# Kernel optimization log

Measured on AMD Instinct MI355X. Metric: run time of the kernel, lower is better.

The kernel has to match this reference:

```python
import jax, jax.numpy as jnp
import numpy as np

B, N, K, D = 8, 4096, 16, 256


def layer_norm(x, g, b, eps=1e-5):
    m = jnp.mean(x, axis=-1, keepdims=True)
    v = jnp.var(x, axis=-1, keepdims=True)
    return (x - m) * jax.lax.rsqrt(v + eps) * g + b


def setup_inputs() -> dict:
    key = jax.random.key(0)
    ks = jax.random.split(key, 8)

    def lin(k, fi, fo):
        return (jax.random.normal(k, (fi, fo), jnp.float32) / np.sqrt(fi).astype(np.float32),
                jnp.zeros((fo,), jnp.float32))

    coordinates = jax.random.normal(ks[0], (B, N, 3), jnp.float32)
    W1, b1 = lin(ks[1], 10, D // 4)
    W2, b2 = lin(ks[2], D // 4, D // 2)
    W3, b3 = lin(ks[3], D // 2, D)
    Wa1, ba1 = lin(ks[4], D, D)
    Wa2, ba2 = lin(ks[5], D, D)
    return {
        'coordinates': coordinates,
        'W1': W1, 'b1': b1, 'g1': jnp.ones((D // 4,)), 'be1': jnp.zeros((D // 4,)),
        'W2': W2, 'b2': b2, 'g2': jnp.ones((D // 2,)), 'be2': jnp.zeros((D // 2,)),
        'W3': W3, 'b3': b3, 'g3': jnp.ones((D,)), 'be3': jnp.zeros((D,)),
        'Wa1': Wa1, 'ba1': ba1, 'ga1': jnp.ones((D,)), 'bea1': jnp.zeros((D,)),
        'Wa2': Wa2, 'ba2': ba2,
    }


def reference(coordinates, W1, b1, g1, be1, W2, b2, g2, be2, W3, b3, g3, be3,
              Wa1, ba1, ga1, bea1, Wa2, ba2):
    # kNN via squared-distance matrix (monotone in Euclidean distance)
    sq = jnp.sum(coordinates * coordinates, axis=-1)  # [B,N]
    d2 = sq[:, :, None] + sq[:, None, :] - 2.0 * jnp.einsum('bnd,bmd->bnm', coordinates, coordinates)
    _, idx = jax.lax.top_k(-d2, K)  # smallest K distances, [B,N,K]

    nbr = jax.vmap(lambda c, i: c[i])(coordinates, idx)  # [B,N,K,3]
    rel = nbr - coordinates[:, :, None, :]               # relative positions
    dist = jnp.linalg.norm(rel, axis=-1, keepdims=True)  # [B,N,K,1]
    rn = rel / (dist + 1e-6)
    axy = jnp.arctan2(rn[..., 1], rn[..., 0])[..., None]
    axz = jnp.arctan2(rn[..., 2], rn[..., 0])[..., None]
    ayz = jnp.arctan2(rn[..., 2], rn[..., 1])[..., None]
    geom = jnp.concatenate([dist, rel, axy, axz, ayz, rn], axis=-1)  # [B,N,K,10]

    # encoder MLP
    h = jax.nn.relu(layer_norm(geom @ W1 + b1, g1, be1))
    h = jax.nn.relu(layer_norm(h @ W2 + b2, g2, be2))
    h = layer_norm(h @ W3 + b3, g3, be3)

    agg = jnp.mean(h, axis=2)  # mean over neighbors -> [B,N,D]

    # aggregator MLP
    out = jax.nn.relu(layer_norm(agg @ Wa1 + ba1, ga1, bea1)) @ Wa2 + ba2
    return out
```

## Files before the change

### kernel.cpp

```cpp
#include <hip/hip_runtime.h>
#include <hip/hip_bf16.h>
#include <math.h>

#define BB 8
#define NN 4096
#define KK 16
#define DD 256

typedef __hip_bfloat16 bf16;
typedef _Float16 half8 __attribute__((ext_vector_type(8)));
typedef float f32x4 __attribute__((ext_vector_type(4)));

union HFU { _Float16 h; unsigned short u; };
__device__ __forceinline__ unsigned short f2h(float x) { HFU v; v.h = (_Float16)x; return v.u; }

#define CONV_TOTAL 273344
#define O_COORD 0
#define O_W1 98304
#define O_b1 98944
#define O_g1 99008
#define O_be1 99072
#define O_W2 99136
#define O_b2 107328
#define O_g2 107456
#define O_be2 107584
#define O_W3 107712
#define O_b3 140480
#define O_g3 140736
#define O_be3 140992
#define O_Wa1 141248
#define O_ba1 206784
#define O_ga1 207040
#define O_bea1 207296
#define O_Wa2 207552
#define O_ba2 273088

#define F_W1 0
#define F_W2 2048
#define F_W3 10240
#define F_A1 43008
#define F_A2 108544
#define FRAG_TOTAL 174080

struct SrcPtrs {
  const void* p[19];
};

__global__ __launch_bounds__(256) void convert_kernel(SrcPtrs sp, float* __restrict__ dst) {
  static constexpr int OFF[20] = {
      0,      98304,  98944,  99008,  99072,  99136,  107328, 107456, 107584,
      107712, 140480, 140736, 140992, 141248, 206784, 207040, 207296, 207552,
      273088, 273344};
  const int i = blockIdx.x * 256 + threadIdx.x;
  if (i >= CONV_TOTAL) return;
  const unsigned tag = ((const unsigned*)sp.p[3])[0];
  const bool isb = (tag == 0x3F803F80u);
  int s = 0;
#pragma unroll
  for (int j = 1; j < 19; j++)
    if (i >= OFF[j]) s = j;
  const int local = i - OFF[s];
  float v = isb ? __bfloat162float(((const bf16*)sp.p[s])[local])
                : ((const float*)sp.p[s])[local];
  dst[i] = v;
}

__global__ __launch_bounds__(256) void swizzle_kernel(const float* __restrict__ conv,
                                                      unsigned short* __restrict__ frag) {
  const int t = blockIdx.x * 256 + threadIdx.x;
  if (t >= FRAG_TOTAL) return;
  int l, e;
  if (t < 2048) { l = 0; e = t; }
  else if (t < 10240) { l = 1; e = t - 2048; }
  else if (t < 43008) { l = 2; e = t - 10240; }
  else if (t < 108544) { l = 3; e = t - 43008; }
  else { l = 4; e = t - 108544; }
  static constexpr int WOFF[5] = {O_W1, O_W2, O_W3, O_Wa1, O_Wa2};
  static constexpr int NDIM[5] = {64, 128, 256, 256, 256};
  static constexpr int NTC[5] = {4, 8, 16, 16, 16};
  static constexpr int KREAL[5] = {10, 64, 128, 256, 256};
  static constexpr int HOFF[5] = {F_W1, F_W2, F_W3, F_A1, F_A2};
  const int j = e & 7;
  const int lane = (e >> 3) & 63;
  const int tile = e >> 9;
  const int nt = tile % NTC[l];
  const int kt = tile / NTC[l];
  const int k = kt * 32 + (lane >> 4) * 8 + j;
  const int n = nt * 16 + (lane & 15);
  float w = (k < KREAL[l]) ? conv[WOFF[l] + k * NDIM[l] + n] : 0.0f;
  frag[HOFF[l] + e] = f2h(w);
}

__device__ __forceinline__ float sq3_rn(float x, float y, float z) {
  return __fadd_rn(__fadd_rn(__fmul_rn(x, x), __fmul_rn(y, y)), __fmul_rn(z, z));
}
__device__ __forceinline__ float dot3_rn(float ax, float ay, float az, float bx, float by, float bz) {
  return __fadd_rn(__fadd_rn(__fmul_rn(ax, bx), __fmul_rn(ay, by)), __fmul_rn(az, bz));
}
__device__ __forceinline__ unsigned f2ord(float f) {
  unsigned u = __float_as_uint(f);
  return (u & 0x80000000u) ? ~u : (u | 0x80000000u);
}
__device__ __forceinline__ float ord2f(unsigned o) {
  unsigned u = (o & 0x80000000u) ? (o & 0x7FFFFFFFu) : ~o;
  return __uint_as_float(u);
}

__device__ __forceinline__ unsigned long long bitonic64(unsigned long long key, int lane) {
#pragma unroll
  for (int k = 2; k <= 64; k <<= 1) {
#pragma unroll
    for (int jj = k >> 1; jj > 0; jj >>= 1) {
      unsigned long long v = __shfl_xor(key, jj, 64);
      bool asc = ((lane & k) == 0);
      bool up = ((lane & jj) != 0);
      unsigned long long mn = (key < v) ? key : v;
      unsigned long long mx2 = (key < v) ? v : key;
      key = (up == asc) ? mx2 : mn;
    }
  }
  return key;
}

__global__ __launch_bounds__(512) void cellsort_kernel(const float* __restrict__ conv,
                                                       float4* __restrict__ sorted,
                                                       int* __restrict__ sidx) {
  __shared__ unsigned hist[512];
  __shared__ unsigned scanb[512];
  const int b = blockIdx.x;
  const int tid = threadIdx.x;
  const float* cb = conv + O_COORD + (size_t)b * NN * 3;
  hist[tid] = 0;
  __syncthreads();
  float xs[8], ys[8], zs[8];
  int cell[8];
  unsigned rank[8];
#pragma unroll
  for (int u = 0; u < 8; u++) {
    int p = u * 512 + tid;
    float x = cb[p * 3 + 0], y = cb[p * 3 + 1], z = cb[p * 3 + 2];
    xs[u] = x; ys[u] = y; zs[u] = z;
    int ix = min(7, max(0, (int)floorf(x + 4.0f)));
    int iy = min(7, max(0, (int)floorf(y + 4.0f)));
    int iz = min(7, max(0, (int)floorf(z + 4.0f)));
    int m = ((ix & 1) | ((ix & 2) << 2) | ((ix & 4) << 4)) |
            (((iy & 1) | ((iy & 2) << 2) | ((iy & 4) << 4)) << 1) |
            (((iz & 1) | ((iz & 2) << 2) | ((iz & 4) << 4)) << 2);
    cell[u] = m;
    rank[u] = atomicAdd(&hist[m], 1u);
  }
  __syncthreads();
  scanb[tid] = hist[tid];
  __syncthreads();
  for (int off = 1; off < 512; off <<= 1) {
    unsigned t = (tid >= off) ? scanb[tid - off] : 0u;
    __syncthreads();
    scanb[tid] += t;
    __syncthreads();
  }
#pragma unroll
  for (int u = 0; u < 8; u++) {
    unsigned base = scanb[cell[u]] - hist[cell[u]];
    unsigned pos = base + rank[u];
    sorted[(size_t)b * NN + pos] =
        make_float4(xs[u], ys[u], zs[u], sq3_rn(xs[u], ys[u], zs[u]));
    sidx[(size_t)b * NN + pos] = u * 512 + tid;
  }
}

__global__ __launch_bounds__(64) void knn_wave_kernel(const float4* __restrict__ soa,
                                                      const int* __restrict__ sI,
                                                      int* __restrict__ idx_out) {
  const int lane = threadIdx.x;
  const int wid = blockIdx.x;
  const int q0 = wid * 4;
  const int b = q0 >> 12;
  const float4* P = soa + (size_t)b * NN;
  const int* I = sI + (size_t)b * NN;
  const int qr = q0 & (NN - 1);
  const int base = qr >> 6;

  float cx[4], cy[4], cz[4], sqn[4];
  int qix[4];
#pragma unroll
  for (int j = 0; j < 4; j++) {
    float4 c = P[qr + j];
    cx[j] = c.x; cy[j] = c.y; cz[j] = c.z; sqn[j] = c.w;
    qix[j] = I[qr + j];
  }

  unsigned long long R[4], pend[4];
  float tauf[4];
  int A[4] = {0, 0, 0, 0};
#pragma unroll
  for (int j = 0; j < 4; j++) pend[j] = ~0ull;

  auto MERGE = [&](int j) {
    unsigned long long key =
        (lane < 16) ? R[j] : ((lane < 16 + A[j]) ? pend[j] : ~0ull);
    key = bitonic64(key, lane);
    R[j] = key;
    tauf[j] = ord2f((unsigned)(unsigned long long)__builtin_amdgcn_readlane(
        (int)(unsigned)(key >> 32), 15));
    A[j] = 0;
  };

  auto APPEND = [&](int j, unsigned long long msk, int cc, unsigned long long key) {
    unsigned rank = __builtin_amdgcn_mbcnt_hi(
        (unsigned)(msk >> 32), __builtin_amdgcn_mbcnt_lo((unsigned)msk, 0u));
    const bool flag = ((msk >> lane) & 1ull) != 0;
    const int lim = 16 + A[j];
    const int nf = lane - (int)rank;
    const int dst = flag ? (lim + (int)rank) : (nf < lim ? nf : nf + cc);
    int src = __builtin_amdgcn_ds_permute(dst << 2, lane) & 63;
    unsigned lo = (unsigned)__builtin_amdgcn_ds_bpermute(src << 2, (int)(unsigned)key);
    unsigned hi = (unsigned)__builtin_amdgcn_ds_bpermute(src << 2, (int)(unsigned)(key >> 32));
    const bool cons = (lane >= lim) && (lane < lim + cc);
    if (cons) pend[j] = (((unsigned long long)hi) << 32) | lo;
    A[j] += cc;
  };

  const int b0 = base * 64 + lane;
  float4 f0 = P[b0];
  int i0 = I[b0];
  const int b1 = ((base + 1) & 63) * 64 + lane;
  float4 f1 = P[b1];
  int i1 = I[b1];
  const int b2i = ((base + 2) & 63) * 64 + lane;
  float4 f2 = P[b2i];
  int i2 = I[b2i];

#pragma unroll
  for (int j = 0; j < 4; j++) {
    float dot = dot3_rn(cx[j], cy[j], cz[j], f0.x, f0.y, f0.z);
    float d2 = __fsub_rn(__fadd_rn(sqn[j], f0.w), __fmul_rn(2.0f, dot));
    unsigned long long key =
        (((unsigned long long)f2ord(d2)) << 32) | (unsigned)i0;
    key = bitonic64(key, lane);
    R[j] = key;
    tauf[j] = ord2f((unsigned)(unsigned long long)__builtin_amdgcn_readlane(
        (int)(unsigned)(key >> 32), 15));
  }

  for (int t = 1; t < 64; t++) {
    const float4 c = f1;
    const int iv = i1;
    f1 = f2; i1 = i2;
    if (t + 2 < 64) {
      const int nb = ((base + t + 2) & 63) * 64 + lane;
      f2 = P[nb];
      i2 = I[nb];
    }
    float d2v[4];
    unsigned long long pm[4];
#pragma unroll
    for (int j = 0; j < 4; j++) {
      float dot = dot3_rn(cx[j], cy[j], cz[j], c.x, c.y, c.z);
      d2v[j] = __fsub_rn(__fadd_rn(sqn[j], c.w), __fmul_rn(2.0f, dot));
      pm[j] = __ballot(d2v[j] <= tauf[j]);
    }
    if (!(pm[0] | pm[1] | pm[2] | pm[3])) continue;
#pragma unroll
    for (int j = 0; j < 4; j++) {
      unsigned long long rem = pm[j];
      if (!rem) continue;
      const unsigned long long key =
          (((unsigned long long)f2ord(d2v[j])) << 32) | (unsigned)iv;
      int cc = __builtin_popcountll(rem);
      while (A[j] + cc > 48) {
        if (A[j] == 0) {
          unsigned long long take = rem & 0xFFFFFFFFull;
          APPEND(j, take, __builtin_popcountll(take), key);
          rem ^= take;
        }
        MERGE(j);
        rem &= __ballot(d2v[j] <= tauf[j]);
        cc = __builtin_popcountll(rem);
      }
      if (cc) APPEND(j, rem, cc, key);
    }
  }

#pragma unroll
  for (int j = 0; j < 4; j++) {
    if (A[j]) MERGE(j);
    if (lane < KK)
      idx_out[((size_t)b * NN + (unsigned)qix[j]) * KK + lane] =
          (int)(R[j] & 0xFFFFFFFFull);
  }
}

template <int KT>
__device__ __forceinline__ void load_afrags(half8* A, const unsigned short* lF,
                                            int rowe, int lane) {
#pragma unroll
  for (int kt = 0; kt < KT; kt++) {
    int off = (lane & 15) * rowe + kt * 32 + (lane >> 4) * 8;
    A[kt] = *reinterpret_cast<const half8*>(lF + off);
  }
}

template <int NT>
__device__ __forceinline__ void init_acc(f32x4* acc, const float* __restrict__ bias,
                                         int lane) {
  const int col = lane & 15;
#pragma unroll
  for (int nt = 0; nt < NT; nt++) {
    float bv = bias[nt * 16 + col];
    acc[nt] = {bv, bv, bv, bv};
  }
}

template <int KT, int NT>
__device__ __forceinline__ void gemm_acc(f32x4* acc, const half8* A,
                                         const unsigned short* bb, int lane) {
#pragma unroll
  for (int kt = 0; kt < KT; kt++)
#pragma unroll
    for (int nt = 0; nt < NT; nt++) {
      const half8 bf = *reinterpret_cast<const half8*>(bb + (kt * NT + nt) * 512 + lane * 8);
      acc[nt] = __builtin_amdgcn_mfma_f32_16x16x32_f16(A[kt], bf, acc[nt], 0, 0, 0);
    }
}

template <int NT>
__device__ __forceinline__ void ln_stats(const f32x4* acc, float* m, float* rs) {
  float s[4] = {0.f, 0.f, 0.f, 0.f}, s2[4] = {0.f, 0.f, 0.f, 0.f};
#pragma unroll
  for (int nt = 0; nt < NT; nt++)
#pragma unroll
    for (int r = 0; r < 4; r++) {
      float v = acc[nt][r];
      s[r] += v;
      s2[r] += v * v;
    }
#pragma unroll
  for (int msk = 1; msk <= 8; msk <<= 1)
#pragma unroll
    for (int r = 0; r < 4; r++) {
      s[r] += __shfl_xor(s[r], msk, 64);
      s2[r] += __shfl_xor(s2[r], msk, 64);
    }
  const float invN = 1.0f / (NT * 16);
#pragma unroll
  for (int r = 0; r < 4; r++) {
    m[r] = s[r] * invN;
    float var = s2[r] * invN - m[r] * m[r];
    rs[r] = rsqrtf(var + 1e-5f);
  }
}

template <int NT, bool RELU>
__device__ __forceinline__ void ln_store(const f32x4* acc, const float* m, const float* rs,
                                         const float* __restrict__ g, const float* __restrict__ be,
                                         unsigned short* lF, int rowe, int lane) {
  const int col = lane & 15;
  const int rbase = (lane >> 4) * 4;
#pragma unroll
  for (int nt = 0; nt < NT; nt++) {
    float gv = g[nt * 16 + col], bv = be[nt * 16 + col];
#pragma unroll
    for (int r = 0; r < 4; r++) {
      float v = (acc[nt][r] - m[r]) * rs[r] * gv + bv;
      if (RELU) v = fmaxf(v, 0.0f);
      lF[(rbase + r) * rowe + nt * 16 + col] = f2h(v);
    }
  }
}

__device__ __forceinline__ void stage_b(unsigned short* bbuf,
                                        const unsigned short* __restrict__ src,
                                        int n_u4, int tid) {
  const uint4* s = reinterpret_cast<const uint4*>(src);
  uint4* d = reinterpret_cast<uint4*>(bbuf);
  for (int i = tid; i < n_u4; i += 256) d[i] = s[i];
}

#define ROWE_E 136
#define PSTR_E (16 * ROWE_E)

__global__ __launch_bounds__(256, 3) void encoder_mfma(
    const float* __restrict__ conv, const int* __restrict__ nbr,
    const unsigned short* __restrict__ frag, unsigned short* __restrict__ agF) {
  __shared__ unsigned short planes[4 * PSTR_E];
  __shared__ unsigned short Bbuf[10240];
  const int tid = threadIdx.x;
  const int lane = tid & 63;
  const int wave = tid >> 6;
  const int point = blockIdx.x * 4 + wave;
  const int b = point >> 12;
  const int n = point & (NN - 1);
  const float* cb = conv + O_COORD + (size_t)b * NN * 3;
  unsigned short* lF = planes + wave * PSTR_E;
  const int g = lane >> 4;
  const int col = lane & 15;

  {
    int pl = tid >> 6, row = (tid >> 2) & 15, part = tid & 3;
    *reinterpret_cast<uint4*>(planes + pl * PSTR_E + row * ROWE_E + part * 8) =
        make_uint4(0u, 0u, 0u, 0u);
    stage_b(Bbuf, frag + F_W1, 1280, tid);
  }
  __syncthreads();

  if (lane < 16) {
    float cx = cb[n * 3 + 0], cy = cb[n * 3 + 1], cz = cb[n * 3 + 2];
    int id = nbr[(size_t)point * KK + lane];
    float rx = __fsub_rn(cb[id * 3 + 0], cx);
    float ry = __fsub_rn(cb[id * 3 + 1], cy);
    float rz = __fsub_rn(cb[id * 3 + 2], cz);
    float dist = __fsqrt_rn(sq3_rn(rx, ry, rz));
    float den = __fadd_rn(dist, 1e-6f);
    float ux = __fdiv_rn(rx, den), uy = __fdiv_rn(ry, den), uz = __fdiv_rn(rz, den);
    float ge[10];
    ge[0] = dist; ge[1] = rx; ge[2] = ry; ge[3] = rz;
    ge[4] = atan2f(uy, ux); ge[5] = atan2f(uz, ux); ge[6] = atan2f(uz, uy);
    ge[7] = ux; ge[8] = uy; ge[9] = uz;
#pragma unroll
    for (int c = 0; c < 10; c++) lF[lane * ROWE_E + c] = f2h(ge[c]);
  }

  {
    half8 x0;
    load_afrags<1>(&x0, lF, ROWE_E, lane);
    f32x4 a1[4];
#pragma unroll
    for (int m = 0; m < 4; m++) {
      const float4 bv = *reinterpret_cast<const float4*>(conv + O_b1 + m * 16 + g * 4);
      a1[m] = {bv.x, bv.y, bv.z, bv.w};
      const half8 wf = *reinterpret_cast<const half8*>(Bbuf + m * 512 + lane * 8);
      a1[m] = __builtin_amdgcn_mfma_f32_16x16x32_f16(wf, x0, a1[m], 0, 0, 0);
    }
    float s = 0.f, s2 = 0.f;
#pragma unroll
    for (int m = 0; m < 4; m++)
#pragma unroll
      for (int r = 0; r < 4; r++) { float v = a1[m][r]; s += v; s2 += v * v; }
    s += __shfl_xor(s, 16, 64); s += __shfl_xor(s, 32, 64);
    s2 += __shfl_xor(s2, 16, 64); s2 += __shfl_xor(s2, 32, 64);
    const float mu = s * (1.0f / 64.0f);
    const float rsg = rsqrtf(s2 * (1.0f / 64.0f) - mu * mu + 1e-5f);
#pragma unroll
    for (int m = 0; m < 4; m++) {
      const float4 gv = *reinterpret_cast<const float4*>(conv + O_g1 + m * 16 + g * 4);
      const float4 bev = *reinterpret_cast<const float4*>(conv + O_be1 + m * 16 + g * 4);
      unsigned long long pk = 0;
#pragma unroll
      for (int r = 0; r < 4; r++) {
        float v = fmaxf((a1[m][r] - mu) * rsg * (&gv.x)[r] + (&bev.x)[r], 0.0f);
        pk |= ((unsigned long long)f2h(v)) << (16 * r);
      }
      *reinterpret_cast<unsigned long long*>(lF + col * ROWE_E + m * 16 + g * 4) = pk;
    }
  }

  {
    half8 x2[2];
    load_afrags<2>(x2, lF, ROWE_E, lane);
    f32x4 a2[8];
#pragma unroll
    for (int m = 0; m < 8; m++) {
      const float4 bv = *reinterpret_cast<const float4*>(conv + O_b2 + m * 16 + g * 4);
      a2[m] = {bv.x, bv.y, bv.z, bv.w};
    }
#pragma unroll
    for (int kt = 0; kt < 2; kt++)
#pragma unroll
      for (int m = 0; m < 8; m++) {
        const half8 wf =
            *reinterpret_cast<const half8*>(Bbuf + 2048 + (kt * 8 + m) * 512 + lane * 8);
        a2[m] = __builtin_amdgcn_mfma_f32_16x16x32_f16(wf, x2[kt], a2[m], 0, 0, 0);
      }
    float s = 0.f, s2 = 0.f;
#pragma unroll
    for (int m = 0; m < 8; m++)
#pragma unroll
      for (int r = 0; r < 4; r++) { float v = a2[m][r]; s += v; s2 += v * v; }
    s += __shfl_xor(s, 16, 64); s += __shfl_xor(s, 32, 64);
    s2 += __shfl_xor(s2, 16, 64); s2 += __shfl_xor(s2, 32, 64);
    const float mu = s * (1.0f / 128.0f);
    const float rsg = rsqrtf(s2 * (1.0f / 128.0f) - mu * mu + 1e-5f);
#pragma unroll
    for (int m = 0; m < 8; m++) {
      const float4 gv = *reinterpret_cast<const float4*>(conv + O_g2 + m * 16 + g * 4);
      const float4 bev = *reinterpret_cast<const float4*>(conv + O_be2 + m * 16 + g * 4);
      unsigned long long pk = 0;
#pragma unroll
      for (int r = 0; r < 4; r++) {
        float v = fmaxf((a2[m][r] - mu) * rsg * (&gv.x)[r] + (&bev.x)[r], 0.0f);
        pk |= ((unsigned long long)f2h(v)) << (16 * r);
      }
      *reinterpret_cast<unsigned long long*>(lF + col * ROWE_E + m * 16 + g * 4) = pk;
    }
  }

  half8 A3[4];
  load_afrags<4>(A3, lF, ROWE_E, lane);
  f32x4 acc[16];
  init_acc<16>(acc, conv + O_b3, lane);
  {
    const unsigned short* W3 = frag + F_W3;
#pragma unroll
    for (int kt = 0; kt < 4; kt++)
#pragma unroll
      for (int nt = 0; nt < 16; nt++) {
        const half8 bf =
            *reinterpret_cast<const half8*>(W3 + (kt * 16 + nt) * 512 + lane * 8);
        acc[nt] = __builtin_amdgcn_mfma_f32_16x16x32_f16(A3[kt], bf, acc[nt], 0, 0, 0);
      }
  }

  {
    float m[4], rs[4];
    ln_stats<16>(acc, m, rs);
    float sv[16];
#pragma unroll
    for (int nt = 0; nt < 16; nt++) {
      float gvv = conv[O_g3 + nt * 16 + col], bvv = conv[O_be3 + nt * 16 + col];
      float s = 0.f;
#pragma unroll
      for (int r = 0; r < 4; r++) s += (acc[nt][r] - m[r]) * rs[r] * gvv + bvv;
      s += __shfl_xor(s, 16, 64);
      s += __shfl_xor(s, 32, 64);
      sv[nt] = s * (1.0f / 16.0f);
    }
    if (lane < 16) {
      size_t base = (size_t)point * DD;
#pragma unroll
      for (int nt = 0; nt < 16; nt++) agF[base + nt * 16 + lane] = f2h(sv[nt]);
    }
  }
}

#define ROWE_A 264

__global__ __launch_bounds__(256) void aggmlp_mfma(
    const float* __restrict__ conv, const unsigned short* __restrict__ agF,
    const unsigned short* __restrict__ a1, const unsigned short* __restrict__ a2,
    const unsigned* __restrict__ g1raw, void* __restrict__ out) {
  __shared__ unsigned short lds[4][16 * ROWE_A];
  const int lane = threadIdx.x & 63;
  const int wave = threadIdx.x >> 6;
  const int row0 = (blockIdx.x * 4 + wave) * 16;
  unsigned short* lF = lds[wave];

#pragma unroll
  for (int t = 0; t < 8; t++) {
    int v = t * 64 + lane;
    int row = v >> 5;
    int c0 = (v & 31) * 8;
    *reinterpret_cast<uint4*>(lF + row * ROWE_A + c0) =
        *reinterpret_cast<const uint4*>(agF + ((size_t)(row0 + row) * DD + c0));
  }
  __syncthreads();

  float m[4], rs[4];
  f32x4 acc[16];
  {
    half8 A[8];
    load_afrags<8>(A, lF, ROWE_A, lane);
    init_acc<16>(acc, conv + O_ba1, lane);
    gemm_acc<8, 16>(acc, A, a1, lane);
    ln_stats<16>(acc, m, rs);
    ln_store<16, true>(acc, m, rs, conv + O_ga1, conv + O_bea1, lF, ROWE_A, lane);
  }
  __syncthreads();
  {
    half8 A[8];
    load_afrags<8>(A, lF, ROWE_A, lane);
    init_acc<16>(acc, conv + O_ba2, lane);
    gemm_acc<8, 16>(acc, A, a2, lane);
  }
  const bool isb = (g1raw[0] == 0x3F803F80u);
  const int col = lane & 15;
  const int rbase = (lane >> 4) * 4;
  if (isb) {
    bf16* o = (bf16*)out;
#pragma unroll
    for (int nt = 0; nt < 16; nt++)
#pragma unroll
      for (int r = 0; r < 4; r++)
        o[(size_t)(row0 + rbase + r) * DD + nt * 16 + col] = __float2bfloat16(acc[nt][r]);
  } else {
    float* o = (float*)out;
#pragma unroll
    for (int nt = 0; nt < 16; nt++)
#pragma unroll
      for (int r = 0; r < 4; r++)
        o[(size_t)(row0 + rbase + r) * DD + nt * 16 + col] = acc[nt][r];
  }
}

extern "C" void kernel_launch(void* const* d_in, const int* in_sizes, int n_in,
                              void* d_out, int out_size, void* d_ws, size_t ws_size,
                              hipStream_t stream) {
  char* ws = (char*)d_ws;
  float* conv = (float*)ws;
  int* idx_ws = (int*)(ws + 1093376);
  unsigned short* agF = (unsigned short*)(ws + 3190528);
  unsigned short* frag = (unsigned short*)(ws + 19967744);
  float4* sorted = (float4*)(ws + 20315904);
  int* sidx = (int*)(ws + 20840192);

  SrcPtrs sp;
  for (int i = 0; i < 19; i++) sp.p[i] = d_in[i];

  convert_kernel<<<(CONV_TOTAL + 255) / 256, 256, 0, stream>>>(sp, conv);
  swizzle_kernel<<<(FRAG_TOTAL + 255) / 256, 256, 0, stream>>>(conv, frag);
  cellsort_kernel<<<BB, 512, 0, stream>>>(conv, sorted, sidx);

  knn_wave_kernel<<<BB * NN / 4, 64, 0, stream>>>(sorted, sidx, idx_ws);

  encoder_mfma<<<BB * NN / 4, 256, 0, stream>>>(conv, idx_ws, frag, agF);

  aggmlp_mfma<<<BB * NN / 64, 256, 0, stream>>>(conv, agF, frag + F_A1, frag + F_A2,
                                                (const unsigned*)d_in[3], d_out);
}
```

Before: 382.5 us.

## Spread geometry atan2 work across all lanes and raise encoder occupancy

The per-neighbor geometry computation previously ran on only 16 of 64 lanes, each doing three atan2 calls serially. Now all 64 lanes run it: each group of 16 lanes computes one of the three angles, and the fourth group writes the distance, relative and unit-vector features. This shortens the serial transcendental chain, at the cost of redundant loads and divisions. Launch bounds go from 3 to 4 blocks per CU, which may force register spills, and the fp16 packing is rewritten with 32-bit words.

```diff
diff --git a/kernel.cpp b/kernel.cpp
--- a/kernel.cpp
+++ b/kernel.cpp
@@ -379,7 +379,7 @@
 #define ROWE_E 136
 #define PSTR_E (16 * ROWE_E)
 
-__global__ __launch_bounds__(256, 3) void encoder_mfma(
+__global__ __launch_bounds__(256, 4) void encoder_mfma(
     const float* __restrict__ conv, const int* __restrict__ nbr,
     const unsigned short* __restrict__ frag, unsigned short* __restrict__ agF) {
   __shared__ unsigned short planes[4 * PSTR_E];
@@ -403,21 +403,27 @@
   }
   __syncthreads();
 
-  if (lane < 16) {
-    float cx = cb[n * 3 + 0], cy = cb[n * 3 + 1], cz = cb[n * 3 + 2];
-    int id = nbr[(size_t)point * KK + lane];
-    float rx = __fsub_rn(cb[id * 3 + 0], cx);
-    float ry = __fsub_rn(cb[id * 3 + 1], cy);
-    float rz = __fsub_rn(cb[id * 3 + 2], cz);
+  {
+    const int nb = col;
+    const int part = g;
+    float cxq = cb[n * 3 + 0], cyq = cb[n * 3 + 1], czq = cb[n * 3 + 2];
+    int id = nbr[(size_t)point * KK + nb];
+    float rx = __fsub_rn(cb[id * 3 + 0], cxq);
+    float ry = __fsub_rn(cb[id * 3 + 1], cyq);
+    float rz = __fsub_rn(cb[id * 3 + 2], czq);
     float dist = __fsqrt_rn(sq3_rn(rx, ry, rz));
     float den = __fadd_rn(dist, 1e-6f);
     float ux = __fdiv_rn(rx, den), uy = __fdiv_rn(ry, den), uz = __fdiv_rn(rz, den);
-    float ge[10];
-    ge[0] = dist; ge[1] = rx; ge[2] = ry; ge[3] = rz;
-    ge[4] = atan2f(uy, ux); ge[5] = atan2f(uz, ux); ge[6] = atan2f(uz, uy);
-    ge[7] = ux; ge[8] = uy; ge[9] = uz;
-#pragma unroll
-    for (int c = 0; c < 10; c++) lF[lane * ROWE_E + c] = f2h(ge[c]);
+    float ya = (part == 0) ? uy : uz;
+    float xa = (part == 2) ? uy : ux;
+    float ang = atan2f(ya, xa);
+    if (part < 3) {
+      lF[nb * ROWE_E + 4 + part] = f2h(ang);
+    } else {
+      unsigned short* r0 = lF + nb * ROWE_E;
+      r0[0] = f2h(dist); r0[1] = f2h(rx); r0[2] = f2h(ry); r0[3] = f2h(rz);
+      r0[7] = f2h(ux); r0[8] = f2h(uy); r0[9] = f2h(uz);
+    }
   }
 
   {
@@ -444,13 +450,14 @@
     for (int m = 0; m < 4; m++) {
       const float4 gv = *reinterpret_cast<const float4*>(conv + O_g1 + m * 16 + g * 4);
       const float4 bev = *reinterpret_cast<const float4*>(conv + O_be1 + m * 16 + g * 4);
-      unsigned long long pk = 0;
-#pragma unroll
-      for (int r = 0; r < 4; r++) {
-        float v = fmaxf((a1[m][r] - mu) * rsg * (&gv.x)[r] + (&bev.x)[r], 0.0f);
-        pk |= ((unsigned long long)f2h(v)) << (16 * r);
-      }
-      *reinterpret_cast<unsigned long long*>(lF + col * ROWE_E + m * 16 + g * 4) = pk;
+      float v0 = fmaxf((a1[m][0] - mu) * rsg * gv.x + bev.x, 0.0f);
+      float v1 = fmaxf((a1[m][1] - mu) * rsg * gv.y + bev.y, 0.0f);
+      float v2 = fmaxf((a1[m][2] - mu) * rsg * gv.z + bev.z, 0.0f);
+      float v3 = fmaxf((a1[m][3] - mu) * rsg * gv.w + bev.w, 0.0f);
+      uint2 pk;
+      pk.x = (unsigned)f2h(v0) | ((unsigned)f2h(v1) << 16);
+      pk.y = (unsigned)f2h(v2) | ((unsigned)f2h(v3) << 16);
+      *reinterpret_cast<uint2*>(lF + col * ROWE_E + m * 16 + g * 4) = pk;
     }
   }
 
@@ -484,13 +491,14 @@
     for (int m = 0; m < 8; m++) {
       const float4 gv = *reinterpret_cast<const float4*>(conv + O_g2 + m * 16 + g * 4);
       const float4 bev = *reinterpret_cast<const float4*>(conv + O_be2 + m * 16 + g * 4);
-      unsigned long long pk = 0;
-#pragma unroll
-      for (int r = 0; r < 4; r++) {
-        float v = fmaxf((a2[m][r] - mu) * rsg * (&gv.x)[r] + (&bev.x)[r], 0.0f);
-        pk |= ((unsigned long long)f2h(v)) << (16 * r);
-      }
-      *reinterpret_cast<unsigned long long*>(lF + col * ROWE_E + m * 16 + g * 4) = pk;
+      float v0 = fmaxf((a2[m][0] - mu) * rsg * gv.x + bev.x, 0.0f);
+      float v1 = fmaxf((a2[m][1] - mu) * rsg * gv.y + bev.y, 0.0f);
+      float v2 = fmaxf((a2[m][2] - mu) * rsg * gv.z + bev.z, 0.0f);
+      float v3 = fmaxf((a2[m][3] - mu) * rsg * gv.w + bev.w, 0.0f);
+      uint2 pk;
+      pk.x = (unsigned)f2h(v0) | ((unsigned)f2h(v1) << 16);
+      pk.y = (unsigned)f2h(v2) | ((unsigned)f2h(v3) << 16);
+      *reinterpret_cast<uint2*>(lF + col * ROWE_E + m * 16 + g * 4) = pk;
     }
   }
 
```

Result: no change. 389.8 us (+1.9%).
